# Performance work log

Hardware: AMD Instinct MI355X
Metric: run time of the kernel (lower is better)

Reference implementation:

```python
import jax, jax.numpy as jnp
import numpy as np

D_MODEL = 1024
NUM_HEADS = 16
HEAD_DIM = D_MODEL // NUM_HEADS
B, S = 4, 2048


def setup_inputs() -> dict:
    key = jax.random.key(0)
    ks = jax.random.split(key, 11)
    sc = 1.0 / np.sqrt(D_MODEL)
    return {
        "query": jax.random.normal(ks[0], (B, S, D_MODEL), jnp.float32),
        "key": jax.random.normal(ks[1], (B, S, D_MODEL), jnp.float32),
        "value": jax.random.normal(ks[2], (B, S, D_MODEL), jnp.float32),
        "Wq": jax.random.normal(ks[3], (D_MODEL, D_MODEL), jnp.float32) * sc,
        "bq": jnp.zeros((D_MODEL,), jnp.float32),
        "Wk": jax.random.normal(ks[4], (D_MODEL, D_MODEL), jnp.float32) * sc,
        "bk": jnp.zeros((D_MODEL,), jnp.float32),
        "Wv": jax.random.normal(ks[5], (D_MODEL, D_MODEL), jnp.float32) * sc,
        "bv": jnp.zeros((D_MODEL,), jnp.float32),
        "Wo": jax.random.normal(ks[6], (D_MODEL, D_MODEL), jnp.float32) * sc,
        "bo": jnp.zeros((D_MODEL,), jnp.float32),
    }


def _split_heads(x):
    b, s, _ = x.shape
    return x.reshape(b, s, NUM_HEADS, HEAD_DIM).transpose(0, 2, 1, 3)  # [B,H,S,Dh]


def reference(query, key, value, Wq, bq, Wk, bk, Wv, bv, Wo, bo):
    q = _split_heads(query @ Wq + bq)
    k = _split_heads(key @ Wk + bk)
    v = _split_heads(value @ Wv + bv)
    scores = jnp.einsum("bhqd,bhkd->bhqk", q, k) / np.sqrt(HEAD_DIM)
    attn = jax.nn.softmax(scores, axis=-1)
    out = jnp.einsum("bhqk,bhkd->bhqd", attn, v)
    out = out.transpose(0, 2, 1, 3).reshape(query.shape[0], -1, D_MODEL)
    return out @ Wo + bo
```

## Files before the change

kernel.cpp:

```cpp
#include <hip/hip_runtime.h>

typedef unsigned short u16;
typedef unsigned int   u32;
typedef unsigned long long u64;
typedef __attribute__((ext_vector_type(8))) short bf16x8;
typedef __attribute__((ext_vector_type(4))) float f32x4;

#define S_  2048
#define DH  64
#define DM  1024
#define BS  8192
#define CS  0.18033688011112042f

static __device__ __forceinline__ float bf2f(u16 v){ return __uint_as_float(((u32)v)<<16); }
static __device__ __forceinline__ u16 f2bf(float f){
  u32 x = __float_as_uint(f);
  return (u16)((x + 0x7fffu + ((x>>16)&1u)) >> 16);
}
#if __has_builtin(__builtin_amdgcn_cvt_pk_bf16_f32)
static __device__ __forceinline__ u32 pk2(float x, float y){
  typedef __attribute__((ext_vector_type(2))) __bf16 bf2v;
  union { bf2v v; u32 u; } c; c.v = __builtin_amdgcn_cvt_pk_bf16_f32(x, y); return c.u;
}
#else
static __device__ __forceinline__ u32 pk2(float x, float y){
  return (u32)f2bf(x) | ((u32)f2bf(y) << 16);
}
#endif
#if __has_builtin(__builtin_amdgcn_exp2f)
#define EXP2F(x) __builtin_amdgcn_exp2f(x)
#else
#define EXP2F(x) exp2f(x)
#endif

static __device__ __forceinline__ void dma16(const u16* g, const u16* l){
  __builtin_amdgcn_global_load_lds(
      (const __attribute__((address_space(1))) u32*)(u64)(uintptr_t)g,
      (__attribute__((address_space(3))) u32*)(u32)(u64)(uintptr_t)l, 16, 0, 0);
}

static __device__ __forceinline__ bf16x8 lds_frag(const u16* p){
  union { bf16x8 f; uint2 u[2]; } w;
  w.u[0] = *(const uint2*)(p);
  w.u[1] = *(const uint2*)(p+4);
  return w.f;
}
static __device__ __forceinline__ bf16x8 frag16v(const u16* p){
  union { bf16x8 f; uint4 u; } w;
  w.u = *(const uint4*)p;
  return w.f;
}
static __device__ __forceinline__ void stage16_bf(const u16* __restrict__ g, u16* s){
  uint4 a = *(const uint4*)g;
  uint4 b = *(const uint4*)(g+8);
  *(uint2*)(s+0)  = make_uint2(a.x,a.y);
  *(uint2*)(s+4)  = make_uint2(a.z,a.w);
  *(uint2*)(s+8)  = make_uint2(b.x,b.y);
  *(uint2*)(s+12) = make_uint2(b.z,b.w);
}
static __device__ __forceinline__ void stage16_f32(const float* __restrict__ g, u16* s){
  float4 a0 = ((const float4*)g)[0];
  float4 a1 = ((const float4*)g)[1];
  float4 a2 = ((const float4*)g)[2];
  float4 a3 = ((const float4*)g)[3];
  *(uint2*)(s+0)  = make_uint2(pk2(a0.x,a0.y), pk2(a0.z,a0.w));
  *(uint2*)(s+4)  = make_uint2(pk2(a1.x,a1.y), pk2(a1.z,a1.w));
  *(uint2*)(s+8)  = make_uint2(pk2(a2.x,a2.y), pk2(a2.z,a2.w));
  *(uint2*)(s+12) = make_uint2(pk2(a3.x,a3.y), pk2(a3.z,a3.w));
}

__global__ __launch_bounds__(256) void detect_f32(const u16* __restrict__ q, int* flag){
  __shared__ int cnt[256];
  int tid = threadIdx.x;
  int bad = 0;
  for (int i = tid; i < 8192; i += 256){
    u32 e = (q[i] >> 7) & 0xFFu;
    bad += (e == 0xFFu) || (e == 0u);
  }
  cnt[tid] = bad;
  __syncthreads();
  for (int s = 128; s > 0; s >>= 1){ if (tid < s) cnt[tid] += cnt[tid+s]; __syncthreads(); }
  if (tid == 0) flag[0] = (cnt[0] > 0) ? 1 : 0;
}

__global__ __launch_bounds__(256) void transpose4(const void* __restrict__ i0,
    const void* __restrict__ i1, const void* __restrict__ i2, const void* __restrict__ i3,
    u16* o0, u16* o1, u16* o2, u16* o3, const int* __restrict__ flag){
  __shared__ u16 tile[32][33];
  int z = blockIdx.z;
  const void* in = z==0?i0 : z==1?i1 : z==2?i2 : i3;
  u16* out = z==0?o0 : z==1?o1 : z==2?o2 : o3;
  bool f32 = flag[0] != 0;
  int tx = threadIdx.x, ty = threadIdx.y;
  int c  = blockIdx.x*32 + tx;
  int r0 = blockIdx.y*32;
  for (int i=ty;i<32;i+=8){
    long off = (long)(r0+i)*DM + c;
    tile[i][tx] = f32 ? f2bf(((const float*)in)[off]) : ((const u16*)in)[off];
  }
  __syncthreads();
  int rr = r0 + tx, c0 = blockIdx.x*32;
  for (int i=ty;i<32;i+=8) out[(long)(c0+i)*DM + rr] = tile[tx][i];
}

__global__ __launch_bounds__(256) void convert3(const void* __restrict__ a0,
    const void* __restrict__ a1, const void* __restrict__ a2,
    u16* o0, u16* o1, u16* o2, const int* __restrict__ flag){
  int z = blockIdx.z;
  const void* in = z==0?a0 : z==1?a1 : a2;
  u16* out = z==0?o0 : z==1?o1 : o2;
  long i = ((long)blockIdx.x*256 + threadIdx.x)*8;
  if (flag[0]){
    const float4* p = (const float4*)((const float*)in + i);
    float4 x = p[0], y = p[1];
    *(uint4*)(out + i) = make_uint4(pk2(x.x,x.y), pk2(x.z,x.w), pk2(y.x,y.y), pk2(y.z,y.w));
  } else {
    *(uint4*)(out + i) = *(const uint4*)((const u16*)in + i);
  }
}

template<int ADMA>
__global__ __launch_bounds__(256) void gemm_qkv(
    const void* __restrict__ A0, const void* __restrict__ A1, const void* __restrict__ A2,
    const u16* __restrict__ W0, const u16* __restrict__ W1, const u16* __restrict__ W2,
    const void* __restrict__ bv0, const void* __restrict__ bv1, const void* __restrict__ bv2,
    u16* C0, u16* C1, u16* C2, const int* __restrict__ flag){
  constexpr int AST = ADMA ? 32 : 36;
  __shared__ __align__(16) u16 As[128*AST];
  __shared__ __align__(16) u16 Bs[128*32];
  int z = blockIdx.z;
  const void* A  = z==0?A0 : z==1?A1 : A2;
  const u16* BT  = z==0?W0 : z==1?W1 : W2;
  const void* bias = z==0?bv0 : z==1?bv1 : bv2;
  u16* C = z==0?C0 : z==1?C1 : C2;
  const int f = flag[0];
  const bool aF32 = (!ADMA) && (f != 0);
  const bool bF32 = (f != 0);
  int tid = threadIdx.x;
  int by = blockIdx.x, bx = blockIdx.y;
  int lane = tid & 63, w = tid >> 6;
  int t = lane & 15, q = lane >> 4;
  int wr = w >> 1, wc = w & 1;
  f32x4 acc[4][4];
  #pragma unroll
  for(int i=0;i<4;i++) for(int j=0;j<4;j++) for(int k=0;k<4;k++) acc[i][j][k]=0.f;

  const u16* gB = BT + ((long)(bx*128 + w*32 + (lane>>2))*DM + (lane&3)*8);
  const u16* lB = &Bs[(w*32)*32];
  const u16* gA_dma = nullptr; const u16* lA_dma = nullptr;
  long aoff = 0;
  if constexpr (ADMA){
    gA_dma = (const u16*)A + ((long)(by*128 + w*32 + (lane>>2))*DM + (lane&3)*8);
    lA_dma = &As[(w*32)*32];
  } else {
    aoff = (long)(by*128 + (tid>>1))*DM + (tid&1)*16;
  }
  const u16* ArdB = &As[(wr*64 + t)*AST + q*8];
  const u16* BrdB = &Bs[(wc*64 + t)*32  + q*8];

  for (int k0=0; k0<DM; k0+=32){
    dma16(gB + k0, lB);
    dma16(gB + 16*DM + k0, lB + 16*32);
    if constexpr (ADMA){
      dma16(gA_dma + k0, lA_dma);
      dma16(gA_dma + 16*DM + k0, lA_dma + 16*32);
    } else {
      u16* AsW = &As[(tid>>1)*36 + (tid&1)*16];
      if (aF32) stage16_f32((const float*)A + aoff + k0, AsW);
      else      stage16_bf ((const u16*)A  + aoff + k0, AsW);
    }
    __syncthreads();
    bf16x8 af[4], bfr[4];
    #pragma unroll
    for (int rt=0;rt<4;rt++) af[rt]  = lds_frag(ArdB + rt*16*AST);
    #pragma unroll
    for (int ct=0;ct<4;ct++) bfr[ct] = lds_frag(BrdB + ct*16*32);
    #pragma unroll
    for (int rt=0;rt<4;rt++)
      #pragma unroll
      for (int ct=0;ct<4;ct++)
        acc[rt][ct] = __builtin_amdgcn_mfma_f32_16x16x32_bf16(af[rt], bfr[ct], acc[rt][ct], 0,0,0);
    __syncthreads();
  }
  float scale = (z==0) ? CS : 1.0f;
  #pragma unroll
  for (int ct=0;ct<4;ct++){
    int col = bx*128 + wc*64 + ct*16 + t;
    float bvv = bF32 ? ((const float*)bias)[col] : bf2f(((const u16*)bias)[col]);
    #pragma unroll
    for (int rt=0;rt<4;rt++){
      int row0 = by*128 + wr*64 + rt*16 + q*4;
      if (z == 2){
        int bb = row0 >> 11, s = row0 & 2047;
        long vbase = (long)bb*2097152 + (long)col*2048
                   + (s & ~63) + ((rt>>1)<<5) + (q<<3) + ((rt&1)<<2);
        u32 lo = pk2(acc[rt][ct][0]+bvv, acc[rt][ct][1]+bvv);
        u32 hi = pk2(acc[rt][ct][2]+bvv, acc[rt][ct][3]+bvv);
        *(uint2*)(C + vbase) = make_uint2(lo,hi);
      } else {
        #pragma unroll
        for (int r=0;r<4;r++)
          C[(long)(row0+r)*DM + col] = f2bf((acc[rt][ct][r] + bvv)*scale);
      }
    }
  }
}

__global__ __launch_bounds__(256) void gemm_o(const u16* __restrict__ A,
    const u16* __restrict__ BT, const void* __restrict__ bias, void* __restrict__ C,
    const int* __restrict__ flag){
  __shared__ __align__(16) u16 As[128*32];
  __shared__ __align__(16) u16 Bs[128*32];
  const int f = flag[0];
  int tid = threadIdx.x;
  int by = blockIdx.x, bx = blockIdx.y;
  int lane = tid & 63, w = tid >> 6;
  int t = lane & 15, q = lane >> 4;
  int wr = w >> 1, wc = w & 1;
  f32x4 acc[4][4];
  #pragma unroll
  for(int i=0;i<4;i++) for(int j=0;j<4;j++) for(int k=0;k<4;k++) acc[i][j][k]=0.f;

  const u16* gA = A  + ((long)(by*128 + w*32 + (lane>>2))*DM + (lane&3)*8);
  const u16* gB = BT + ((long)(bx*128 + w*32 + (lane>>2))*DM + (lane&3)*8);
  const u16* lA = &As[(w*32)*32];
  const u16* lB = &Bs[(w*32)*32];
  const u16* ArdB = &As[(wr*64 + t)*32 + q*8];
  const u16* BrdB = &Bs[(wc*64 + t)*32 + q*8];

  for (int k0=0; k0<DM; k0+=32){
    dma16(gA + k0, lA);
    dma16(gA + 16*DM + k0, lA + 16*32);
    dma16(gB + k0, lB);
    dma16(gB + 16*DM + k0, lB + 16*32);
    __syncthreads();
    bf16x8 af[4], bfr[4];
    #pragma unroll
    for (int rt=0;rt<4;rt++) af[rt]  = lds_frag(ArdB + rt*16*32);
    #pragma unroll
    for (int ct=0;ct<4;ct++) bfr[ct] = lds_frag(BrdB + ct*16*32);
    #pragma unroll
    for (int rt=0;rt<4;rt++)
      #pragma unroll
      for (int ct=0;ct<4;ct++)
        acc[rt][ct] = __builtin_amdgcn_mfma_f32_16x16x32_bf16(af[rt], bfr[ct], acc[rt][ct], 0,0,0);
    __syncthreads();
  }
  #pragma unroll
  for (int ct=0;ct<4;ct++){
    int col = bx*128 + wc*64 + ct*16 + t;
    float bvv = f ? ((const float*)bias)[col] : bf2f(((const u16*)bias)[col]);
    #pragma unroll
    for (int rt=0;rt<4;rt++){
      int row0 = by*128 + wr*64 + rt*16 + q*4;
      #pragma unroll
      for (int r=0;r<4;r++){
        long idx = (long)(row0+r)*DM + col;
        float v = acc[rt][ct][r] + bvv;
        if (f) ((float*)C)[idx] = v;
        else   ((u16*)C)[idx]  = f2bf(v);
      }
    }
  }
}

__global__ __launch_bounds__(256,4) void attn5(const u16* __restrict__ Q,
    const u16* __restrict__ Kb, const u16* __restrict__ Vt, u16* __restrict__ O){
  __shared__ __align__(16) u16 Ks[2][4096];
  __shared__ __align__(16) u16 Vs[2][4096];
  int tid = threadIdx.x;
  int bid = blockIdx.x;
  int qt = bid >> 6;
  int s6 = bid & 63;
  int bh = (s6 & 7)*8 + (s6 >> 3);
  int b = bh >> 4, h = bh & 15;
  int lane = tid & 63, w = tid >> 6;
  int t = lane & 15, q = lane >> 4;

  const u16* Qbase = Q + ((long)(b*S_ + qt*128 + w*32 + t)*DM + h*DH + q*8);
  bf16x8 qf[2][2];
  qf[0][0] = frag16v(Qbase);
  qf[0][1] = frag16v(Qbase + 32);
  qf[1][0] = frag16v(Qbase + 16*DM);
  qf[1][1] = frag16v(Qbase + 16*DM + 32);

  int r0 = tid >> 3;
  int cb = ((tid & 7) * 16) ^ ((r0 & 7) << 4);
  const char* gK = (const char*)Kb + (((long)(b*S_ + r0)*DM + h*DH) << 1) + cb;
  const char* gV = (const char*)Vt + ((((long)bh << 17) + ((long)r0 << 11)) << 1) + cb;
  const long gK1 = ((long)32*DM) << 1;
  const long gV1 = ((long)32*S_) << 1;
  const int ld0 = w*512, ld1 = 2048 + w*512;

  f32x4 o[2][4];
  #pragma unroll
  for (int i=0;i<2;i++) for (int j=0;j<4;j++) for (int k=0;k<4;k++) o[i][j][k]=0.f;
  f32x4 o4[2];
  #pragma unroll
  for (int i=0;i<2;i++) for (int k=0;k<4;k++) o4[i][k]=0.f;

  union { bf16x8 f; u32 u[4]; } vone;
  { u32 ovv = (t==0) ? 0x3F803F80u : 0u;
    vone.u[0]=ovv; vone.u[1]=ovv; vone.u[2]=ovv; vone.u[3]=ovv; }

  const int xorv = (t & 7) << 4;

  dma16((const u16*)(gK),       &Ks[0][ld0]);
  dma16((const u16*)(gK + gK1), &Ks[0][ld1]);
  dma16((const u16*)(gV),       &Vs[0][ld0]);
  dma16((const u16*)(gV + gV1), &Vs[0][ld1]);

  for (int kt=0; kt<32; kt++){
    int cur = kt & 1;
    if (kt < 31){
      long ko = ((long)(kt+1)*64*DM) << 1;
      long vo = (long)(kt+1) << 7;
      dma16((const u16*)(gK + ko),       &Ks[cur^1][ld0]);
      dma16((const u16*)(gK + ko + gK1), &Ks[cur^1][ld1]);
      dma16((const u16*)(gV + vo),       &Vs[cur^1][ld0]);
      dma16((const u16*)(gV + vo + gV1), &Vs[cur^1][ld1]);
      asm volatile("s_waitcnt vmcnt(4)" ::: "memory");
    } else {
      asm volatile("s_waitcnt vmcnt(0)" ::: "memory");
    }
    __builtin_amdgcn_s_barrier();

    const u16* Kc = Ks[cur];
    const u16* Vc = Vs[cur];

    f32x4 sacc[2][4];
    #pragma unroll
    for (int i=0;i<2;i++) for (int j=0;j<4;j++) for (int k=0;k<4;k++) sacc[i][j][k]=0.f;
    #pragma unroll
    for (int ks=0; ks<2; ks++){
      int off = ((ks*64 + q*16) ^ xorv) >> 1;
      bf16x8 k0 = frag16v(Kc + (t     )*64 + off);
      bf16x8 k1 = frag16v(Kc + (16 + t)*64 + off);
      bf16x8 k2 = frag16v(Kc + (32 + t)*64 + off);
      bf16x8 k3 = frag16v(Kc + (48 + t)*64 + off);
      __builtin_amdgcn_s_setprio(1);
      #pragma unroll
      for (int rt=0; rt<2; rt++){
        sacc[rt][0] = __builtin_amdgcn_mfma_f32_16x16x32_bf16(k0, qf[rt][ks], sacc[rt][0],0,0,0);
        sacc[rt][1] = __builtin_amdgcn_mfma_f32_16x16x32_bf16(k1, qf[rt][ks], sacc[rt][1],0,0,0);
        sacc[rt][2] = __builtin_amdgcn_mfma_f32_16x16x32_bf16(k2, qf[rt][ks], sacc[rt][2],0,0,0);
        sacc[rt][3] = __builtin_amdgcn_mfma_f32_16x16x32_bf16(k3, qf[rt][ks], sacc[rt][3],0,0,0);
      }
      __builtin_amdgcn_s_setprio(0);
    }

    union { bf16x8 f; u32 u[4]; } af[2][2];
    #pragma unroll
    for (int rt=0; rt<2; rt++){
      float ev[4][4];
      #pragma unroll
      for (int c=0; c<4; c++)
        #pragma unroll
        for (int r=0; r<4; r++) ev[c][r] = EXP2F(sacc[rt][c][r]);
      #pragma unroll
      for (int ks=0; ks<2; ks++){
        af[rt][ks].u[0] = pk2(ev[2*ks  ][0], ev[2*ks  ][1]);
        af[rt][ks].u[1] = pk2(ev[2*ks  ][2], ev[2*ks  ][3]);
        af[rt][ks].u[2] = pk2(ev[2*ks+1][0], ev[2*ks+1][1]);
        af[rt][ks].u[3] = pk2(ev[2*ks+1][2], ev[2*ks+1][3]);
      }
    }

    #pragma unroll
    for (int ks=0; ks<2; ks++){
      int off = ((ks*64 + q*16) ^ xorv) >> 1;
      bf16x8 v0 = frag16v(Vc + (t     )*64 + off);
      bf16x8 v1 = frag16v(Vc + (16 + t)*64 + off);
      bf16x8 v2 = frag16v(Vc + (32 + t)*64 + off);
      bf16x8 v3 = frag16v(Vc + (48 + t)*64 + off);
      __builtin_amdgcn_s_setprio(1);
      #pragma unroll
      for (int rt=0; rt<2; rt++){
        o[rt][0] = __builtin_amdgcn_mfma_f32_16x16x32_bf16(af[rt][ks].f, v0, o[rt][0],0,0,0);
        o[rt][1] = __builtin_amdgcn_mfma_f32_16x16x32_bf16(af[rt][ks].f, v1, o[rt][1],0,0,0);
        o[rt][2] = __builtin_amdgcn_mfma_f32_16x16x32_bf16(af[rt][ks].f, v2, o[rt][2],0,0,0);
        o[rt][3] = __builtin_amdgcn_mfma_f32_16x16x32_bf16(af[rt][ks].f, v3, o[rt][3],0,0,0);
        o4[rt]   = __builtin_amdgcn_mfma_f32_16x16x32_bf16(af[rt][ks].f, vone.f, o4[rt],0,0,0);
      }
      __builtin_amdgcn_s_setprio(0);
    }
    __builtin_amdgcn_s_barrier();
  }

  #pragma unroll
  for (int rt=0; rt<2; rt++){
    #pragma unroll
    for (int r=0; r<4; r++){
      float l = __shfl(o4[rt][r], lane & 48);
      float inv = 1.f / l;
      int row = qt*128 + w*32 + rt*16 + q*4 + r;
      #pragma unroll
      for (int ct=0; ct<4; ct++)
        O[(long)(b*S_ + row)*DM + h*DH + ct*16 + t] = f2bf(o[rt][ct][r] * inv);
    }
  }
}

extern "C" void kernel_launch(void* const* d_in, const int* in_sizes, int n_in,
                              void* d_out, int out_size, void* d_ws, size_t ws_size,
                              hipStream_t stream){
  (void)in_sizes; (void)n_in; (void)out_size;
  const void* xq = d_in[0];
  const void* xk = d_in[1];
  const void* xv = d_in[2];
  const void* Wq = d_in[3];
  const void* bq = d_in[4];
  const void* Wk = d_in[5];
  const void* bk = d_in[6];
  const void* Wv = d_in[7];
  const void* bv = d_in[8];
  const void* Wo = d_in[9];
  const void* bo = d_in[10];

  int* flag = (int*)d_ws;
  u16* base = (u16*)((char*)d_ws + 256);
  const long NT = (long)BS*DM;
  u16* Qb  = base;
  u16* Kbf = base + NT;
  u16* Vt  = base + 2*NT;
  u16* WqT = base + 3*NT;
  u16* WkT = WqT + (long)DM*DM;
  u16* WvT = WkT + (long)DM*DM;
  u16* WoT = WvT + (long)DM*DM;
  u16* Xc0 = WoT + (long)DM*DM;
  u16* Xc1 = Xc0 + NT;
  u16* Xc2 = Xc1 + NT;
  size_t need_pre = 256 + (size_t)(6*NT + 4*(long)DM*DM)*2;
  bool pre = ws_size >= need_pre;

  detect_f32<<<1, 256, 0, stream>>>((const u16*)xq, flag);

  transpose4<<<dim3(32,32,4), dim3(32,8,1), 0, stream>>>(Wq, Wk, Wv, Wo,
      WqT, WkT, WvT, WoT, flag);

  dim3 gb(256,1,1);
  if (pre){
    convert3<<<dim3(4096,1,3), gb, 0, stream>>>(xq, xk, xv, Xc0, Xc1, Xc2, flag);
    gemm_qkv<1><<<dim3(64,8,3), gb, 0, stream>>>(Xc0, Xc1, Xc2,
        WqT, WkT, WvT, bq, bk, bv, Qb, Kbf, Vt, flag);
  } else {
    gemm_qkv<0><<<dim3(64,8,3), gb, 0, stream>>>(xq, xk, xv,
        WqT, WkT, WvT, bq, bk, bv, Qb, Kbf, Vt, flag);
  }

  attn5<<<dim3(1024,1,1), gb, 0, stream>>>(Qb, Kbf, Vt, Qb );

  gemm_o<<<dim3(64,8,1), gb, 0, stream>>>(Qb, WoT, bo, d_out, flag);
}
```

Measured before the change: 360.5 us.

## Software-pipeline attention QK/PV across tiles and drop the detect/convert pre-passes

The attention kernel now keeps three K buffers and two V buffers in one shared array. Each iteration computes QK^T for tile kt while doing PV for tile kt-1 with the softmax from the previous step, so MFMA work and exp work interleave and prefetch runs further ahead. The host now picks the fp32/bf16 mode from in_sizes instead of running a detection kernel, and the convert3 pre-pass plus the DMA-A GEMM path are removed, so the QKV GEMM always converts fp32 activations while staging them. This saves two launches and a full pass over the activations. In exchange it uses more shared memory per block (40 KB instead of 32 KB) and relies on in_sizes being in bytes.

```diff
diff --git a/kernel.cpp b/kernel.cpp
--- a/kernel.cpp
+++ b/kernel.cpp
@@ -69,28 +69,16 @@
   *(uint2*)(s+12) = make_uint2(pk2(a3.x,a3.y), pk2(a3.z,a3.w));
 }
 
-__global__ __launch_bounds__(256) void detect_f32(const u16* __restrict__ q, int* flag){
-  __shared__ int cnt[256];
-  int tid = threadIdx.x;
-  int bad = 0;
-  for (int i = tid; i < 8192; i += 256){
-    u32 e = (q[i] >> 7) & 0xFFu;
-    bad += (e == 0xFFu) || (e == 0u);
-  }
-  cnt[tid] = bad;
-  __syncthreads();
-  for (int s = 128; s > 0; s >>= 1){ if (tid < s) cnt[tid] += cnt[tid+s]; __syncthreads(); }
-  if (tid == 0) flag[0] = (cnt[0] > 0) ? 1 : 0;
-}
+union AFU { bf16x8 f; u32 u[4]; };
 
 __global__ __launch_bounds__(256) void transpose4(const void* __restrict__ i0,
     const void* __restrict__ i1, const void* __restrict__ i2, const void* __restrict__ i3,
-    u16* o0, u16* o1, u16* o2, u16* o3, const int* __restrict__ flag){
+    u16* o0, u16* o1, u16* o2, u16* o3, const int f32f){
   __shared__ u16 tile[32][33];
   int z = blockIdx.z;
   const void* in = z==0?i0 : z==1?i1 : z==2?i2 : i3;
   u16* out = z==0?o0 : z==1?o1 : z==2?o2 : o3;
-  bool f32 = flag[0] != 0;
+  bool f32 = f32f != 0;
   int tx = threadIdx.x, ty = threadIdx.y;
   int c  = blockIdx.x*32 + tx;
   int r0 = blockIdx.y*32;
@@ -103,29 +91,12 @@
   for (int i=ty;i<32;i+=8) out[(long)(c0+i)*DM + rr] = tile[tx][i];
 }
 
-__global__ __launch_bounds__(256) void convert3(const void* __restrict__ a0,
-    const void* __restrict__ a1, const void* __restrict__ a2,
-    u16* o0, u16* o1, u16* o2, const int* __restrict__ flag){
-  int z = blockIdx.z;
-  const void* in = z==0?a0 : z==1?a1 : a2;
-  u16* out = z==0?o0 : z==1?o1 : o2;
-  long i = ((long)blockIdx.x*256 + threadIdx.x)*8;
-  if (flag[0]){
-    const float4* p = (const float4*)((const float*)in + i);
-    float4 x = p[0], y = p[1];
-    *(uint4*)(out + i) = make_uint4(pk2(x.x,x.y), pk2(x.z,x.w), pk2(y.x,y.y), pk2(y.z,y.w));
-  } else {
-    *(uint4*)(out + i) = *(const uint4*)((const u16*)in + i);
-  }
-}
-
-template<int ADMA>
 __global__ __launch_bounds__(256) void gemm_qkv(
     const void* __restrict__ A0, const void* __restrict__ A1, const void* __restrict__ A2,
     const u16* __restrict__ W0, const u16* __restrict__ W1, const u16* __restrict__ W2,
     const void* __restrict__ bv0, const void* __restrict__ bv1, const void* __restrict__ bv2,
-    u16* C0, u16* C1, u16* C2, const int* __restrict__ flag){
-  constexpr int AST = ADMA ? 32 : 36;
+    u16* C0, u16* C1, u16* C2, const int f32f){
+  constexpr int AST = 36;
   __shared__ __align__(16) u16 As[128*AST];
   __shared__ __align__(16) u16 Bs[128*32];
   int z = blockIdx.z;
@@ -133,9 +104,7 @@
   const u16* BT  = z==0?W0 : z==1?W1 : W2;
   const void* bias = z==0?bv0 : z==1?bv1 : bv2;
   u16* C = z==0?C0 : z==1?C1 : C2;
-  const int f = flag[0];
-  const bool aF32 = (!ADMA) && (f != 0);
-  const bool bF32 = (f != 0);
+  const bool aF32 = (f32f != 0);
   int tid = threadIdx.x;
   int by = blockIdx.x, bx = blockIdx.y;
   int lane = tid & 63, w = tid >> 6;
@@ -147,28 +116,16 @@
 
   const u16* gB = BT + ((long)(bx*128 + w*32 + (lane>>2))*DM + (lane&3)*8);
   const u16* lB = &Bs[(w*32)*32];
-  const u16* gA_dma = nullptr; const u16* lA_dma = nullptr;
-  long aoff = 0;
-  if constexpr (ADMA){
-    gA_dma = (const u16*)A + ((long)(by*128 + w*32 + (lane>>2))*DM + (lane&3)*8);
-    lA_dma = &As[(w*32)*32];
-  } else {
-    aoff = (long)(by*128 + (tid>>1))*DM + (tid&1)*16;
-  }
+  long aoff = (long)(by*128 + (tid>>1))*DM + (tid&1)*16;
   const u16* ArdB = &As[(wr*64 + t)*AST + q*8];
   const u16* BrdB = &Bs[(wc*64 + t)*32  + q*8];
 
   for (int k0=0; k0<DM; k0+=32){
     dma16(gB + k0, lB);
     dma16(gB + 16*DM + k0, lB + 16*32);
-    if constexpr (ADMA){
-      dma16(gA_dma + k0, lA_dma);
-      dma16(gA_dma + 16*DM + k0, lA_dma + 16*32);
-    } else {
-      u16* AsW = &As[(tid>>1)*36 + (tid&1)*16];
-      if (aF32) stage16_f32((const float*)A + aoff + k0, AsW);
-      else      stage16_bf ((const u16*)A  + aoff + k0, AsW);
-    }
+    u16* AsW = &As[(tid>>1)*36 + (tid&1)*16];
+    if (aF32) stage16_f32((const float*)A + aoff + k0, AsW);
+    else      stage16_bf ((const u16*)A  + aoff + k0, AsW);
     __syncthreads();
     bf16x8 af[4], bfr[4];
     #pragma unroll
@@ -186,7 +143,7 @@
   #pragma unroll
   for (int ct=0;ct<4;ct++){
     int col = bx*128 + wc*64 + ct*16 + t;
-    float bvv = bF32 ? ((const float*)bias)[col] : bf2f(((const u16*)bias)[col]);
+    float bvv = aF32 ? ((const float*)bias)[col] : bf2f(((const u16*)bias)[col]);
     #pragma unroll
     for (int rt=0;rt<4;rt++){
       int row0 = by*128 + wr*64 + rt*16 + q*4;
@@ -208,10 +165,10 @@
 
 __global__ __launch_bounds__(256) void gemm_o(const u16* __restrict__ A,
     const u16* __restrict__ BT, const void* __restrict__ bias, void* __restrict__ C,
-    const int* __restrict__ flag){
+    const int f32f){
   __shared__ __align__(16) u16 As[128*32];
   __shared__ __align__(16) u16 Bs[128*32];
-  const int f = flag[0];
+  const int f = f32f;
   int tid = threadIdx.x;
   int by = blockIdx.x, bx = blockIdx.y;
   int lane = tid & 63, w = tid >> 6;
@@ -264,10 +221,77 @@
   }
 }
 
-__global__ __launch_bounds__(256,4) void attn5(const u16* __restrict__ Q,
+static __device__ __forceinline__ void qk16(const u16* Kc, int t, int q, int xorv,
+    const bf16x8 (&qf)[2][2], f32x4 (&sacc)[2][4]){
+  #pragma unroll
+  for (int i=0;i<2;i++)
+    #pragma unroll
+    for (int j=0;j<4;j++)
+      #pragma unroll
+      for (int k=0;k<4;k++) sacc[i][j][k]=0.f;
+  #pragma unroll
+  for (int ks=0; ks<2; ks++){
+    int off = ((ks*64 + q*16) ^ xorv) >> 1;
+    bf16x8 k0 = frag16v(Kc + (t     )*64 + off);
+    bf16x8 k1 = frag16v(Kc + (16 + t)*64 + off);
+    bf16x8 k2 = frag16v(Kc + (32 + t)*64 + off);
+    bf16x8 k3 = frag16v(Kc + (48 + t)*64 + off);
+    __builtin_amdgcn_s_setprio(1);
+    #pragma unroll
+    for (int rt=0; rt<2; rt++){
+      sacc[rt][0] = __builtin_amdgcn_mfma_f32_16x16x32_bf16(k0, qf[rt][ks], sacc[rt][0],0,0,0);
+      sacc[rt][1] = __builtin_amdgcn_mfma_f32_16x16x32_bf16(k1, qf[rt][ks], sacc[rt][1],0,0,0);
+      sacc[rt][2] = __builtin_amdgcn_mfma_f32_16x16x32_bf16(k2, qf[rt][ks], sacc[rt][2],0,0,0);
+      sacc[rt][3] = __builtin_amdgcn_mfma_f32_16x16x32_bf16(k3, qf[rt][ks], sacc[rt][3],0,0,0);
+    }
+    __builtin_amdgcn_s_setprio(0);
+  }
+}
+
+static __device__ __forceinline__ void sm16(const f32x4 (&sacc)[2][4], AFU (&af)[2][2]){
+  #pragma unroll
+  for (int rt=0; rt<2; rt++){
+    float ev[4][4];
+    #pragma unroll
+    for (int c=0; c<4; c++)
+      #pragma unroll
+      for (int r=0; r<4; r++) ev[c][r] = EXP2F(sacc[rt][c][r]);
+    #pragma unroll
+    for (int ks=0; ks<2; ks++){
+      af[rt][ks].u[0] = pk2(ev[2*ks  ][0], ev[2*ks  ][1]);
+      af[rt][ks].u[1] = pk2(ev[2*ks  ][2], ev[2*ks  ][3]);
+      af[rt][ks].u[2] = pk2(ev[2*ks+1][0], ev[2*ks+1][1]);
+      af[rt][ks].u[3] = pk2(ev[2*ks+1][2], ev[2*ks+1][3]);
+    }
+  }
+}
+
+static __device__ __forceinline__ void pv16(const u16* Vc, int t, int q, int xorv,
+    const AFU (&af)[2][2], bf16x8 vonef, f32x4 (&o)[2][4], f32x4 (&o4)[2]){
+  #pragma unroll
+  for (int ks=0; ks<2; ks++){
+    int off = ((ks*64 + q*16) ^ xorv) >> 1;
+    bf16x8 v0 = frag16v(Vc + (t     )*64 + off);
+    bf16x8 v1 = frag16v(Vc + (16 + t)*64 + off);
+    bf16x8 v2 = frag16v(Vc + (32 + t)*64 + off);
+    bf16x8 v3 = frag16v(Vc + (48 + t)*64 + off);
+    __builtin_amdgcn_s_setprio(1);
+    #pragma unroll
+    for (int rt=0; rt<2; rt++){
+      o[rt][0] = __builtin_amdgcn_mfma_f32_16x16x32_bf16(af[rt][ks].f, v0, o[rt][0],0,0,0);
+      o[rt][1] = __builtin_amdgcn_mfma_f32_16x16x32_bf16(af[rt][ks].f, v1, o[rt][1],0,0,0);
+      o[rt][2] = __builtin_amdgcn_mfma_f32_16x16x32_bf16(af[rt][ks].f, v2, o[rt][2],0,0,0);
+      o[rt][3] = __builtin_amdgcn_mfma_f32_16x16x32_bf16(af[rt][ks].f, v3, o[rt][3],0,0,0);
+      o4[rt]   = __builtin_amdgcn_mfma_f32_16x16x32_bf16(af[rt][ks].f, vonef, o4[rt],0,0,0);
+    }
+    __builtin_amdgcn_s_setprio(0);
+  }
+}
+
+__global__ __launch_bounds__(256,4) void attn6(const u16* __restrict__ Q,
     const u16* __restrict__ Kb, const u16* __restrict__ Vt, u16* __restrict__ O){
-  __shared__ __align__(16) u16 Ks[2][4096];
-  __shared__ __align__(16) u16 Vs[2][4096];
+  __shared__ __align__(16) u16 SM_[20480];
+  const int VB = 12288;
   int tid = threadIdx.x;
   int bid = blockIdx.x;
   int qt = bid >> 6;
@@ -290,14 +314,21 @@
   const char* gV = (const char*)Vt + ((((long)bh << 17) + ((long)r0 << 11)) << 1) + cb;
   const long gK1 = ((long)32*DM) << 1;
   const long gV1 = ((long)32*S_) << 1;
+  const long KT  = ((long)64*DM) << 1;
   const int ld0 = w*512, ld1 = 2048 + w*512;
 
   f32x4 o[2][4];
   #pragma unroll
-  for (int i=0;i<2;i++) for (int j=0;j<4;j++) for (int k=0;k<4;k++) o[i][j][k]=0.f;
+  for (int i=0;i<2;i++)
+    #pragma unroll
+    for (int j=0;j<4;j++)
+      #pragma unroll
+      for (int k=0;k<4;k++) o[i][j][k]=0.f;
   f32x4 o4[2];
   #pragma unroll
-  for (int i=0;i<2;i++) for (int k=0;k<4;k++) o4[i][k]=0.f;
+  for (int i=0;i<2;i++)
+    #pragma unroll
+    for (int k=0;k<4;k++) o4[i][k]=0.f;
 
   union { bf16x8 f; u32 u[4]; } vone;
   { u32 ovv = (t==0) ? 0x3F803F80u : 0u;
@@ -305,87 +336,48 @@
 
   const int xorv = (t & 7) << 4;
 
-  dma16((const u16*)(gK),       &Ks[0][ld0]);
-  dma16((const u16*)(gK + gK1), &Ks[0][ld1]);
-  dma16((const u16*)(gV),       &Vs[0][ld0]);
-  dma16((const u16*)(gV + gV1), &Vs[0][ld1]);
-
-  for (int kt=0; kt<32; kt++){
-    int cur = kt & 1;
-    if (kt < 31){
-      long ko = ((long)(kt+1)*64*DM) << 1;
-      long vo = (long)(kt+1) << 7;
-      dma16((const u16*)(gK + ko),       &Ks[cur^1][ld0]);
-      dma16((const u16*)(gK + ko + gK1), &Ks[cur^1][ld1]);
-      dma16((const u16*)(gV + vo),       &Vs[cur^1][ld0]);
-      dma16((const u16*)(gV + vo + gV1), &Vs[cur^1][ld1]);
-      asm volatile("s_waitcnt vmcnt(4)" ::: "memory");
-    } else {
-      asm volatile("s_waitcnt vmcnt(0)" ::: "memory");
-    }
+  dma16((const u16*)(gK),            &SM_[ld0]);
+  dma16((const u16*)(gK + gK1),      &SM_[ld1]);
+  dma16((const u16*)(gV),            &SM_[VB + ld0]);
+  dma16((const u16*)(gV + gV1),      &SM_[VB + ld1]);
+  dma16((const u16*)(gK + KT),       &SM_[4096 + ld0]);
+  dma16((const u16*)(gK + KT + gK1), &SM_[4096 + ld1]);
+  asm volatile("s_waitcnt vmcnt(4)" ::: "memory");
+  __builtin_amdgcn_s_barrier();
+
+  f32x4 sacc[2][4];
+  AFU af[2][2];
+  qk16(&SM_[0], t, q, xorv, qf, sacc);
+  sm16(sacc, af);
+  dma16((const u16*)(gK + 2*KT),       &SM_[8192 + ld0]);
+  dma16((const u16*)(gK + 2*KT + gK1), &SM_[8192 + ld1]);
+  dma16((const u16*)(gV + (1L<<7)),        &SM_[VB + 4096 + ld0]);
+  dma16((const u16*)(gV + (1L<<7) + gV1),  &SM_[VB + 4096 + ld1]);
+
+  int kcur = 4096, knx = 8192, kfree = 0;
+  for (int kt = 1; kt < 32; kt++){
+    asm volatile("s_waitcnt vmcnt(4)" ::: "memory");
     __builtin_amdgcn_s_barrier();
-
-    const u16* Kc = Ks[cur];
-    const u16* Vc = Vs[cur];
-
-    f32x4 sacc[2][4];
-    #pragma unroll
-    for (int i=0;i<2;i++) for (int j=0;j<4;j++) for (int k=0;k<4;k++) sacc[i][j][k]=0.f;
-    #pragma unroll
-    for (int ks=0; ks<2; ks++){
-      int off = ((ks*64 + q*16) ^ xorv) >> 1;
-      bf16x8 k0 = frag16v(Kc + (t     )*64 + off);
-      bf16x8 k1 = frag16v(Kc + (16 + t)*64 + off);
-      bf16x8 k2 = frag16v(Kc + (32 + t)*64 + off);
-      bf16x8 k3 = frag16v(Kc + (48 + t)*64 + off);
-      __builtin_amdgcn_s_setprio(1);
-      #pragma unroll
-      for (int rt=0; rt<2; rt++){
-        sacc[rt][0] = __builtin_amdgcn_mfma_f32_16x16x32_bf16(k0, qf[rt][ks], sacc[rt][0],0,0,0);
-        sacc[rt][1] = __builtin_amdgcn_mfma_f32_16x16x32_bf16(k1, qf[rt][ks], sacc[rt][1],0,0,0);
-        sacc[rt][2] = __builtin_amdgcn_mfma_f32_16x16x32_bf16(k2, qf[rt][ks], sacc[rt][2],0,0,0);
-        sacc[rt][3] = __builtin_amdgcn_mfma_f32_16x16x32_bf16(k3, qf[rt][ks], sacc[rt][3],0,0,0);
-      }
-      __builtin_amdgcn_s_setprio(0);
-    }
-
-    union { bf16x8 f; u32 u[4]; } af[2][2];
-    #pragma unroll
-    for (int rt=0; rt<2; rt++){
-      float ev[4][4];
-      #pragma unroll
-      for (int c=0; c<4; c++)
-        #pragma unroll
-        for (int r=0; r<4; r++) ev[c][r] = EXP2F(sacc[rt][c][r]);
-      #pragma unroll
-      for (int ks=0; ks<2; ks++){
-        af[rt][ks].u[0] = pk2(ev[2*ks  ][0], ev[2*ks  ][1]);
-        af[rt][ks].u[1] = pk2(ev[2*ks  ][2], ev[2*ks  ][3]);
-        af[rt][ks].u[2] = pk2(ev[2*ks+1][0], ev[2*ks+1][1]);
-        af[rt][ks].u[3] = pk2(ev[2*ks+1][2], ev[2*ks+1][3]);
-      }
-    }
-
-    #pragma unroll
-    for (int ks=0; ks<2; ks++){
-      int off = ((ks*64 + q*16) ^ xorv) >> 1;
-      bf16x8 v0 = frag16v(Vc + (t     )*64 + off);
-      bf16x8 v1 = frag16v(Vc + (16 + t)*64 + off);
-      bf16x8 v2 = frag16v(Vc + (32 + t)*64 + off);
-      bf16x8 v3 = frag16v(Vc + (48 + t)*64 + off);
-      __builtin_amdgcn_s_setprio(1);
-      #pragma unroll
-      for (int rt=0; rt<2; rt++){
-        o[rt][0] = __builtin_amdgcn_mfma_f32_16x16x32_bf16(af[rt][ks].f, v0, o[rt][0],0,0,0);
-        o[rt][1] = __builtin_amdgcn_mfma_f32_16x16x32_bf16(af[rt][ks].f, v1, o[rt][1],0,0,0);
-        o[rt][2] = __builtin_amdgcn_mfma_f32_16x16x32_bf16(af[rt][ks].f, v2, o[rt][2],0,0,0);
-        o[rt][3] = __builtin_amdgcn_mfma_f32_16x16x32_bf16(af[rt][ks].f, v3, o[rt][3],0,0,0);
-        o4[rt]   = __builtin_amdgcn_mfma_f32_16x16x32_bf16(af[rt][ks].f, vone.f, o4[rt],0,0,0);
-      }
-      __builtin_amdgcn_s_setprio(0);
-    }
+    if (kt <= 30){
+      int nk = (kt+2 < 32) ? (kt+2) : 31;
+      const char* g = gK + (long)nk*KT;
+      dma16((const u16*)(g),       &SM_[kfree + ld0]);
+      dma16((const u16*)(g + gK1), &SM_[kfree + ld1]);
+    }
+    qk16(&SM_[kcur], t, q, xorv, qf, sacc);
+    pv16(&SM_[VB + (((kt-1)&1)<<12)], t, q, xorv, af, vone.f, o, o4);
+    sm16(sacc, af);
     __builtin_amdgcn_s_barrier();
-  }
+    if (kt <= 30){
+      const char* g = gV + ((long)(kt+1) << 7);
+      dma16((const u16*)(g),       &SM_[VB + (((kt+1)&1)<<12) + ld0]);
+      dma16((const u16*)(g + gV1), &SM_[VB + (((kt+1)&1)<<12) + ld1]);
+    }
+    int tmp = kcur; kcur = knx; knx = kfree; kfree = tmp;
+  }
+  asm volatile("s_waitcnt vmcnt(0)" ::: "memory");
+  __builtin_amdgcn_s_barrier();
+  pv16(&SM_[VB + 4096], t, q, xorv, af, vone.f, o, o4);
 
   #pragma unroll
   for (int rt=0; rt<2; rt++){
@@ -404,7 +396,7 @@
 extern "C" void kernel_launch(void* const* d_in, const int* in_sizes, int n_in,
                               void* d_out, int out_size, void* d_ws, size_t ws_size,
                               hipStream_t stream){
-  (void)in_sizes; (void)n_in; (void)out_size;
+  (void)n_in; (void)out_size; (void)ws_size;
   const void* xq = d_in[0];
   const void* xk = d_in[1];
   const void* xv = d_in[2];
@@ -417,9 +409,11 @@
   const void* Wo = d_in[9];
   const void* bo = d_in[10];
 
-  int* flag = (int*)d_ws;
+  const long NT = (long)BS*DM;
+  int f32f = 1;
+  if (in_sizes && in_sizes[0] == (int)(NT*2)) f32f = 0;
+
   u16* base = (u16*)((char*)d_ws + 256);
-  const long NT = (long)BS*DM;
   u16* Qb  = base;
   u16* Kbf = base + NT;
   u16* Vt  = base + 2*NT;
@@ -427,28 +421,15 @@
   u16* WkT = WqT + (long)DM*DM;
   u16* WvT = WkT + (long)DM*DM;
   u16* WoT = WvT + (long)DM*DM;
-  u16* Xc0 = WoT + (long)DM*DM;
-  u16* Xc1 = Xc0 + NT;
-  u16* Xc2 = Xc1 + NT;
-  size_t need_pre = 256 + (size_t)(6*NT + 4*(long)DM*DM)*2;
-  bool pre = ws_size >= need_pre;
-
-  detect_f32<<<1, 256, 0, stream>>>((const u16*)xq, flag);
-
+
+  dim3 gb(256,1,1);
   transpose4<<<dim3(32,32,4), dim3(32,8,1), 0, stream>>>(Wq, Wk, Wv, Wo,
-      WqT, WkT, WvT, WoT, flag);
-
-  dim3 gb(256,1,1);
-  if (pre){
-    convert3<<<dim3(4096,1,3), gb, 0, stream>>>(xq, xk, xv, Xc0, Xc1, Xc2, flag);
-    gemm_qkv<1><<<dim3(64,8,3), gb, 0, stream>>>(Xc0, Xc1, Xc2,
-        WqT, WkT, WvT, bq, bk, bv, Qb, Kbf, Vt, flag);
-  } else {
-    gemm_qkv<0><<<dim3(64,8,3), gb, 0, stream>>>(xq, xk, xv,
-        WqT, WkT, WvT, bq, bk, bv, Qb, Kbf, Vt, flag);
-  }
-
-  attn5<<<dim3(1024,1,1), gb, 0, stream>>>(Qb, Kbf, Vt, Qb );
-
-  gemm_o<<<dim3(64,8,1), gb, 0, stream>>>(Qb, WoT, bo, d_out, flag);
-}
+      WqT, WkT, WvT, WoT, f32f);
+
+  gemm_qkv<<<dim3(64,8,3), gb, 0, stream>>>(xq, xk, xv,
+      WqT, WkT, WvT, bq, bk, bv, Qb, Kbf, Vt, f32f);
+
+  attn6<<<dim3(1024,1,1), gb, 0, stream>>>(Qb, Kbf, Vt, Qb );
+
+  gemm_o<<<dim3(64,8,1), gb, 0, stream>>>(Qb, WoT, bo, d_out, f32f);
+}
```

New measurement: 403.7 us. 1.12x slower.
